# Kernel tuning notes

Measured on AMD Instinct MI355X. Metric: run time of the kernel, lower is better.

The kernel has to match this reference:

```python
import jax, jax.numpy as jnp
import numpy as np

D_KEY = 512
D_VALUE = 512
D_MEM_HIDDEN = 64
BATCH = 65536


def setup_inputs() -> dict:
    key = jax.random.key(0)
    ks = jax.random.split(key, 6)
    return {
        "key": jax.random.normal(ks[0], (BATCH, D_KEY), dtype=jnp.float32),
        "value": jax.random.normal(ks[1], (BATCH, D_VALUE), dtype=jnp.float32),
        # memory MLP weights (the stored memory)
        "mem_W1": jax.random.normal(ks[2], (D_MEM_HIDDEN, D_KEY), dtype=jnp.float32) * 0.02,
        "mem_b1": jnp.zeros((D_MEM_HIDDEN,), dtype=jnp.float32),
        "mem_W2": jax.random.normal(ks[3], (D_VALUE, D_MEM_HIDDEN), dtype=jnp.float32) * 0.02,
        "mem_b2": jnp.zeros((D_VALUE,), dtype=jnp.float32),
        # per-dimension precision head
        "prec_W": jax.random.normal(ks[4], (D_VALUE, D_KEY), dtype=jnp.float32) * 0.01,
        "prec_b": jnp.ones((D_VALUE,), dtype=jnp.float32),
    }


def reference(key, value, mem_W1, mem_b1, mem_W2, mem_b2, prec_W, prec_b):
    """Faithful translation of MemoryModule.free_energy.

    F = prec * clamp(value - pred, -3, 3)^2 - log(prec), averaged over d_value.
    """
    # predict: two-layer MLP with exact (erf) GELU, matching torch F.gelu default
    h = jax.nn.gelu(key @ mem_W1.T + mem_b1, approximate=False)  # (B, H)
    pred = h @ mem_W2.T + mem_b2                                  # (B, Dv)
    # precision head: softplus + 0.01, always positive
    prec = jax.nn.softplus(key @ prec_W.T + prec_b) + 0.01        # (B, Dv)
    error = jnp.clip(value - pred, -3.0, 3.0)                     # (B, Dv)
    F_per_dim = prec * error * error - jnp.log(prec)
    F_scalar = F_per_dim.mean(axis=-1)                            # (B,)
    return (F_scalar, pred, prec, error)
```

## Files before the change

kernel.cpp:

```cpp
#include <hip/hip_runtime.h>
#include <hip/hip_bf16.h>

#define BATCH 65536
#define DK 512
#define DV 512
#define DH 64
#define BM 64
#define NT (DV / 16)

typedef __attribute__((ext_vector_type(8))) short bf16x8;
typedef __attribute__((ext_vector_type(4))) float f32x4;

__device__ short g_wb[327680];

__device__ __forceinline__ short f2bf(float f) {
    union { __hip_bfloat16 h; short s; } u;
    u.h = __float2bfloat16(f);
    return u.s;
}

__global__ __launch_bounds__(256) void conv_weights(
    const float* __restrict__ W1, const float* __restrict__ W2,
    const float* __restrict__ Wp)
{
    int t = blockIdx.x * 256 + threadIdx.x;
    long bx = (long)t * 16;
    long inseg; const float* src; int sh;
    if (bx < 65536)       { inseg = bx;          src = W1; sh = 10; }
    else if (bx < 131072) { inseg = bx - 65536;  src = W2; sh = 7;  }
    else                  { inseg = bx - 131072; src = Wp; sh = 10; }
    long so = inseg ^ (((inseg >> sh) & 7) << 4);
    const float* p = src + (so >> 1);
    float4 a = *reinterpret_cast<const float4*>(p);
    float4 b = *reinterpret_cast<const float4*>(p + 4);
    bf16x8 r;
    r[0] = f2bf(a.x); r[1] = f2bf(a.y); r[2] = f2bf(a.z); r[3] = f2bf(a.w);
    r[4] = f2bf(b.x); r[5] = f2bf(b.y); r[6] = f2bf(b.z); r[7] = f2bf(b.w);
    *reinterpret_cast<bf16x8*>(reinterpret_cast<char*>(g_wb) + bx) = r;
}

__device__ __forceinline__ void gld16(const short* g, short* l) {
    __builtin_amdgcn_global_load_lds(
        (const __attribute__((address_space(1))) void*)g,
        (__attribute__((address_space(3))) void*)l, 16, 0, 0);
}

#define WPA 0
#define WPB 16384
#define W2A 32768
#define W2B (32768 + 2048)

__global__ __launch_bounds__(256, 4) void fused_free_energy(
    const float* __restrict__ key, const float* __restrict__ value,
    const float* __restrict__ b1, const float* __restrict__ b2,
    const float* __restrict__ pb,
    float* __restrict__ outF, float* __restrict__ outPred,
    float* __restrict__ outPrec, float* __restrict__ outErr)
{
    __shared__ __align__(16) short ldsS[18432];
    char* ldsb = reinterpret_cast<char*>(ldsS);

    const short* W1b = g_wb;
    const short* W2b = g_wb + 32768;
    const short* Wpb = g_wb + 65536;

    const int tid  = threadIdx.x;
    const int wave = tid >> 6;
    const int lane = tid & 63;
    const int lh   = lane & 15;
    const int lg   = lane >> 4;
    const long row0 = (long)blockIdx.x * BM;

    bf16x8 kreg[16];
    #pragma unroll
    for (int c = 0; c < 2; ++c) {
        const float4* kin = reinterpret_cast<const float4*>(key + (row0 + c * 32) * DK);
        #pragma unroll
        for (int i = 0; i < 16; ++i) {
            int idx = i * 256 + tid;
            int r = idx >> 7, c4 = idx & 127;
            float4 v = kin[idx];
            short4 s;
            s.x = f2bf(v.x); s.y = f2bf(v.y); s.z = f2bf(v.z); s.w = f2bf(v.w);
            int byte = (r * 1024 + c4 * 8) ^ ((r & 7) << 4);
            *reinterpret_cast<short4*>(ldsb + byte) = s;
        }
        __syncthreads();
        if ((wave >> 1) == c) {
            int rr = (wave & 1) * 16 + lh;
            #pragma unroll
            for (int kk = 0; kk < 16; ++kk) {
                int byte = (rr * 1024 + kk * 64 + lg * 16) ^ ((rr & 7) << 4);
                kreg[kk] = *reinterpret_cast<const bf16x8*>(ldsb + byte);
            }
        }
        __syncthreads();
    }

    const f32x4 zf = {0.f, 0.f, 0.f, 0.f};

    short hs_all[16];
    {
        #pragma unroll
        for (int i = 0; i < 4; ++i) {
            int ch = (wave + i * 4) * 1024;
            gld16(W1b + ((ch + lane * 16) >> 1), ldsS + ((WPA + ch) >> 1));
        }
        __syncthreads();
        #pragma unroll
        for (int jt = 0; jt < 4; ++jt) {
            char* cbuf = ldsb + ((jt & 1) ? WPB : WPA);
            if (jt < 3) {
                int nb_ = (jt & 1) ? WPA : WPB;
                #pragma unroll
                for (int i = 0; i < 4; ++i) {
                    int ch = (wave + i * 4) * 1024;
                    gld16(W1b + (((jt + 1) * 16384 + ch + lane * 16) >> 1),
                          ldsS + ((nb_ + ch) >> 1));
                }
            }
            f32x4 acc = zf;
            #pragma unroll
            for (int kk = 0; kk < 16; ++kk) {
                int byte = (lh * 1024 + kk * 64 + lg * 16) ^ ((lh & 7) << 4);
                bf16x8 af = *reinterpret_cast<const bf16x8*>(cbuf + byte);
                acc = __builtin_amdgcn_mfma_f32_16x16x32_bf16(af, kreg[kk], acc, 0, 0, 0);
            }
            float4 b1v = *reinterpret_cast<const float4*>(b1 + jt * 16 + lg * 4);
            float b1a[4] = {b1v.x, b1v.y, b1v.z, b1v.w};
            #pragma unroll
            for (int r = 0; r < 4; ++r) {
                float z = acc[r] + b1a[r];
                float g = 0.5f * z * (1.0f + erff(z * 0.70710678f));
                hs_all[jt * 4 + r] = f2bf(g);
            }
            __syncthreads();
        }
        #pragma unroll
        for (int jt = 0; jt < 4; ++jt) {
            int hb = WPA + wave * 2048 + ((lh * 128 + jt * 32 + lg * 8) ^ ((lh & 7) << 4));
            short4 hv = {hs_all[jt * 4 + 0], hs_all[jt * 4 + 1],
                         hs_all[jt * 4 + 2], hs_all[jt * 4 + 3]};
            *reinterpret_cast<short4*>(ldsb + hb) = hv;
        }
        __syncthreads();
    }

    bf16x8 hreg[2];
    #pragma unroll
    for (int kh = 0; kh < 2; ++kh) {
        int byte = (lh * 128 + kh * 64 + lg * 16) ^ ((lh & 7) << 4);
        hreg[kh] = *reinterpret_cast<const bf16x8*>(ldsb + WPA + wave * 2048 + byte);
    }
    __syncthreads();

    {
        #pragma unroll
        for (int i = 0; i < 4; ++i) {
            int ch = (wave + i * 4) * 1024;
            gld16(Wpb + ((ch + lane * 16) >> 1), ldsS + ((WPA + ch) >> 1));
        }
        if (wave < 2)
            gld16(W2b + ((wave * 1024 + lane * 16) >> 1), ldsS + ((W2A + wave * 1024) >> 1));
        __syncthreads();

        float facc = 0.f;
        const long grow = row0 + wave * 16 + lh;
        const float* vrow = value + grow * DV;
        float* prow = outPred + grow * DV;
        float* crow = outPrec + grow * DV;
        float* erow = outErr  + grow * DV;

        for (int it = 0; it < NT; ++it) {
            char* wpc = ldsb + ((it & 1) ? WPB : WPA);
            char* w2c = ldsb + ((it & 1) ? W2B : W2A);

            if (it + 1 < NT) {
                int nwp = (it & 1) ? WPA : WPB;
                int nw2 = (it & 1) ? W2A : W2B;
                #pragma unroll
                for (int i = 0; i < 4; ++i) {
                    int ch = (wave + i * 4) * 1024;
                    gld16(Wpb + (((it + 1) * 16384 + ch + lane * 16) >> 1),
                          ldsS + ((nwp + ch) >> 1));
                }
                if (wave < 2)
                    gld16(W2b + (((it + 1) * 2048 + wave * 1024 + lane * 16) >> 1),
                          ldsS + ((nw2 + wave * 1024) >> 1));
            }

            f32x4 acc3 = zf;
            #pragma unroll
            for (int kk = 0; kk < 16; ++kk) {
                int byte = (lh * 1024 + kk * 64 + lg * 16) ^ ((lh & 7) << 4);
                bf16x8 af = *reinterpret_cast<const bf16x8*>(wpc + byte);
                acc3 = __builtin_amdgcn_mfma_f32_16x16x32_bf16(af, kreg[kk], acc3, 0, 0, 0);
            }
            f32x4 acc2 = zf;
            #pragma unroll
            for (int kh = 0; kh < 2; ++kh) {
                int byte = (lh * 128 + kh * 64 + lg * 16) ^ ((lh & 7) << 4);
                bf16x8 af = *reinterpret_cast<const bf16x8*>(w2c + byte);
                acc2 = __builtin_amdgcn_mfma_f32_16x16x32_bf16(af, hreg[kh], acc2, 0, 0, 0);
            }

            int nb = it * 16 + lg * 4;
            float4 b2v = *reinterpret_cast<const float4*>(b2 + nb);
            float4 pbv = *reinterpret_cast<const float4*>(pb + nb);
            float4 val = *reinterpret_cast<const float4*>(vrow + nb);
            float b2a[4] = {b2v.x, b2v.y, b2v.z, b2v.w};
            float pba[4] = {pbv.x, pbv.y, pbv.z, pbv.w};
            float va[4]  = {val.x, val.y, val.z, val.w};
            float prv[4], pcv[4], erv[4];
            #pragma unroll
            for (int r = 0; r < 4; ++r) {
                float pred = acc2[r] + b2a[r];
                float z    = acc3[r] + pba[r];
                float prec = fmaxf(z, 0.f) + __logf(1.0f + __expf(-fabsf(z))) + 0.01f;
                float err  = fminf(fmaxf(va[r] - pred, -3.f), 3.f);
                prv[r] = pred; pcv[r] = prec; erv[r] = err;
                facc += prec * err * err - __logf(prec);
            }
            float4 pr4 = {prv[0], prv[1], prv[2], prv[3]};
            float4 pc4 = {pcv[0], pcv[1], pcv[2], pcv[3]};
            float4 er4 = {erv[0], erv[1], erv[2], erv[3]};
            *reinterpret_cast<float4*>(prow + nb) = pr4;
            *reinterpret_cast<float4*>(crow + nb) = pc4;
            *reinterpret_cast<float4*>(erow + nb) = er4;

            __syncthreads();
        }

        facc += __shfl_xor(facc, 16, 64);
        facc += __shfl_xor(facc, 32, 64);
        if (lane < 16) outF[grow] = facc * (1.0f / 512.0f);
    }
}

extern "C" void kernel_launch(void* const* d_in, const int* in_sizes, int n_in,
                              void* d_out, int out_size, void* d_ws, size_t ws_size,
                              hipStream_t stream) {
    const float* key   = (const float*)d_in[0];
    const float* value = (const float*)d_in[1];
    const float* W1    = (const float*)d_in[2];
    const float* b1    = (const float*)d_in[3];
    const float* W2    = (const float*)d_in[4];
    const float* b2    = (const float*)d_in[5];
    const float* Wp    = (const float*)d_in[6];
    const float* pb    = (const float*)d_in[7];

    float* outF    = (float*)d_out;
    float* outPred = outF + BATCH;
    float* outPrec = outPred + (long)BATCH * DV;
    float* outErr  = outPrec + (long)BATCH * DV;

    conv_weights<<<160, 256, 0, stream>>>(W1, W2, Wp);
    fused_free_energy<<<BATCH / BM, 256, 0, stream>>>(key, value, b1, b2, pb,
                                                      outF, outPred, outPrec, outErr);
}
```

Before: 289.3 us.

## Read bf16 weights directly from global/L2 instead of staging through LDS

The weight-staging pipeline through LDS is removed. Each wave now loads W1, Wp and W2 bf16 fragments straight from global memory, relying on L2/cache hits because every block shares the weights. This drops the per-iteration __syncthreads and the swizzled weight layout. Key rows are loaded directly into registers, the next value tile is prefetched, and the MFMA chains are split into two accumulators. Occupancy is lowered to 3 blocks per CU, and the change risks heavier global/L1 traffic since each wave re-fetches the weights independently.

```diff
diff --git a/kernel.cpp b/kernel.cpp
--- a/kernel.cpp
+++ b/kernel.cpp
@@ -11,7 +11,7 @@
 typedef __attribute__((ext_vector_type(8))) short bf16x8;
 typedef __attribute__((ext_vector_type(4))) float f32x4;
 
-__device__ short g_wb[327680];
+__device__ __align__(16) short g_wb[327680];
 
 __device__ __forceinline__ short f2bf(float f) {
     union { __hip_bfloat16 h; short s; } u;
@@ -19,46 +19,37 @@
     return u.s;
 }
 
+__device__ __forceinline__ bf16x8 pack8(float4 a, float4 b) {
+    bf16x8 r;
+    r[0] = f2bf(a.x); r[1] = f2bf(a.y); r[2] = f2bf(a.z); r[3] = f2bf(a.w);
+    r[4] = f2bf(b.x); r[5] = f2bf(b.y); r[6] = f2bf(b.z); r[7] = f2bf(b.w);
+    return r;
+}
+
 __global__ __launch_bounds__(256) void conv_weights(
     const float* __restrict__ W1, const float* __restrict__ W2,
     const float* __restrict__ Wp)
 {
     int t = blockIdx.x * 256 + threadIdx.x;
-    long bx = (long)t * 16;
-    long inseg; const float* src; int sh;
-    if (bx < 65536)       { inseg = bx;          src = W1; sh = 10; }
-    else if (bx < 131072) { inseg = bx - 65536;  src = W2; sh = 7;  }
-    else                  { inseg = bx - 131072; src = Wp; sh = 10; }
-    long so = inseg ^ (((inseg >> sh) & 7) << 4);
-    const float* p = src + (so >> 1);
-    float4 a = *reinterpret_cast<const float4*>(p);
-    float4 b = *reinterpret_cast<const float4*>(p + 4);
-    bf16x8 r;
-    r[0] = f2bf(a.x); r[1] = f2bf(a.y); r[2] = f2bf(a.z); r[3] = f2bf(a.w);
-    r[4] = f2bf(b.x); r[5] = f2bf(b.y); r[6] = f2bf(b.z); r[7] = f2bf(b.w);
-    *reinterpret_cast<bf16x8*>(reinterpret_cast<char*>(g_wb) + bx) = r;
+    long e = (long)t * 8;
+    const float* src; long off;
+    if (e < 32768)      { src = W1; off = e; }
+    else if (e < 65536) { src = W2; off = e - 32768; }
+    else                { src = Wp; off = e - 65536; }
+    float4 a = *reinterpret_cast<const float4*>(src + off);
+    float4 b = *reinterpret_cast<const float4*>(src + off + 4);
+    *reinterpret_cast<bf16x8*>(g_wb + e) = pack8(a, b);
 }
 
-__device__ __forceinline__ void gld16(const short* g, short* l) {
-    __builtin_amdgcn_global_load_lds(
-        (const __attribute__((address_space(1))) void*)g,
-        (__attribute__((address_space(3))) void*)l, 16, 0, 0);
-}
-
-#define WPA 0
-#define WPB 16384
-#define W2A 32768
-#define W2B (32768 + 2048)
-
-__global__ __launch_bounds__(256, 4) void fused_free_energy(
+__global__ __launch_bounds__(256, 3) void fused_free_energy(
     const float* __restrict__ key, const float* __restrict__ value,
     const float* __restrict__ b1, const float* __restrict__ b2,
     const float* __restrict__ pb,
     float* __restrict__ outF, float* __restrict__ outPred,
     float* __restrict__ outPrec, float* __restrict__ outErr)
 {
-    __shared__ __align__(16) short ldsS[18432];
-    char* ldsb = reinterpret_cast<char*>(ldsS);
+    __shared__ __align__(16) short hpark[4096];
+    char* hpb = reinterpret_cast<char*>(hpark);
 
     const short* W1b = g_wb;
     const short* W2b = g_wb + 32768;
@@ -70,100 +61,56 @@
     const int lh   = lane & 15;
     const int lg   = lane >> 4;
     const long row0 = (long)blockIdx.x * BM;
+    const f32x4 zf = {0.f, 0.f, 0.f, 0.f};
 
     bf16x8 kreg[16];
-    #pragma unroll
-    for (int c = 0; c < 2; ++c) {
-        const float4* kin = reinterpret_cast<const float4*>(key + (row0 + c * 32) * DK);
+    {
+        const float* krow = key + (row0 + wave * 16 + lh) * DK + lg * 8;
         #pragma unroll
-        for (int i = 0; i < 16; ++i) {
-            int idx = i * 256 + tid;
-            int r = idx >> 7, c4 = idx & 127;
-            float4 v = kin[idx];
-            short4 s;
-            s.x = f2bf(v.x); s.y = f2bf(v.y); s.z = f2bf(v.z); s.w = f2bf(v.w);
-            int byte = (r * 1024 + c4 * 8) ^ ((r & 7) << 4);
-            *reinterpret_cast<short4*>(ldsb + byte) = s;
+        for (int kk = 0; kk < 16; ++kk) {
+            float4 a = *reinterpret_cast<const float4*>(krow + kk * 32);
+            float4 b = *reinterpret_cast<const float4*>(krow + kk * 32 + 4);
+            kreg[kk] = pack8(a, b);
         }
-        __syncthreads();
-        if ((wave >> 1) == c) {
-            int rr = (wave & 1) * 16 + lh;
-            #pragma unroll
-            for (int kk = 0; kk < 16; ++kk) {
-                int byte = (rr * 1024 + kk * 64 + lg * 16) ^ ((rr & 7) << 4);
-                kreg[kk] = *reinterpret_cast<const bf16x8*>(ldsb + byte);
-            }
-        }
-        __syncthreads();
     }
 
-    const f32x4 zf = {0.f, 0.f, 0.f, 0.f};
-
     short hs_all[16];
-    {
+    #pragma unroll
+    for (int jt = 0; jt < 4; ++jt) {
+        const short* wt = W1b + (jt * 16 + lh) * DK + lg * 8;
+        f32x4 aE = zf, aO = zf;
         #pragma unroll
-        for (int i = 0; i < 4; ++i) {
-            int ch = (wave + i * 4) * 1024;
-            gld16(W1b + ((ch + lane * 16) >> 1), ldsS + ((WPA + ch) >> 1));
+        for (int kk = 0; kk < 16; kk += 2) {
+            bf16x8 f0 = *reinterpret_cast<const bf16x8*>(wt + kk * 32);
+            bf16x8 f1 = *reinterpret_cast<const bf16x8*>(wt + kk * 32 + 32);
+            aE = __builtin_amdgcn_mfma_f32_16x16x32_bf16(f0, kreg[kk],     aE, 0, 0, 0);
+            aO = __builtin_amdgcn_mfma_f32_16x16x32_bf16(f1, kreg[kk + 1], aO, 0, 0, 0);
         }
-        __syncthreads();
+        float4 b1v = *reinterpret_cast<const float4*>(b1 + jt * 16 + lg * 4);
+        float b1a[4] = {b1v.x, b1v.y, b1v.z, b1v.w};
         #pragma unroll
-        for (int jt = 0; jt < 4; ++jt) {
-            char* cbuf = ldsb + ((jt & 1) ? WPB : WPA);
-            if (jt < 3) {
-                int nb_ = (jt & 1) ? WPA : WPB;
-                #pragma unroll
-                for (int i = 0; i < 4; ++i) {
-                    int ch = (wave + i * 4) * 1024;
-                    gld16(W1b + (((jt + 1) * 16384 + ch + lane * 16) >> 1),
-                          ldsS + ((nb_ + ch) >> 1));
-                }
-            }
-            f32x4 acc = zf;
-            #pragma unroll
-            for (int kk = 0; kk < 16; ++kk) {
-                int byte = (lh * 1024 + kk * 64 + lg * 16) ^ ((lh & 7) << 4);
-                bf16x8 af = *reinterpret_cast<const bf16x8*>(cbuf + byte);
-                acc = __builtin_amdgcn_mfma_f32_16x16x32_bf16(af, kreg[kk], acc, 0, 0, 0);
-            }
-            float4 b1v = *reinterpret_cast<const float4*>(b1 + jt * 16 + lg * 4);
-            float b1a[4] = {b1v.x, b1v.y, b1v.z, b1v.w};
-            #pragma unroll
-            for (int r = 0; r < 4; ++r) {
-                float z = acc[r] + b1a[r];
-                float g = 0.5f * z * (1.0f + erff(z * 0.70710678f));
-                hs_all[jt * 4 + r] = f2bf(g);
-            }
-            __syncthreads();
+        for (int r = 0; r < 4; ++r) {
+            float z = aE[r] + aO[r] + b1a[r];
+            float g = 0.5f * z * (1.0f + erff(z * 0.70710678f));
+            hs_all[jt * 4 + r] = f2bf(g);
         }
-        #pragma unroll
-        for (int jt = 0; jt < 4; ++jt) {
-            int hb = WPA + wave * 2048 + ((lh * 128 + jt * 32 + lg * 8) ^ ((lh & 7) << 4));
-            short4 hv = {hs_all[jt * 4 + 0], hs_all[jt * 4 + 1],
-                         hs_all[jt * 4 + 2], hs_all[jt * 4 + 3]};
-            *reinterpret_cast<short4*>(ldsb + hb) = hv;
-        }
-        __syncthreads();
     }
-
+    #pragma unroll
+    for (int jt = 0; jt < 4; ++jt) {
+        int hb = wave * 2048 + ((lh * 128 + jt * 32 + lg * 8) ^ ((lh & 7) << 4));
+        short4 hv = {hs_all[jt * 4 + 0], hs_all[jt * 4 + 1],
+                     hs_all[jt * 4 + 2], hs_all[jt * 4 + 3]};
+        *reinterpret_cast<short4*>(hpb + hb) = hv;
+    }
+    __syncthreads();
     bf16x8 hreg[2];
     #pragma unroll
     for (int kh = 0; kh < 2; ++kh) {
         int byte = (lh * 128 + kh * 64 + lg * 16) ^ ((lh & 7) << 4);
-        hreg[kh] = *reinterpret_cast<const bf16x8*>(ldsb + WPA + wave * 2048 + byte);
+        hreg[kh] = *reinterpret_cast<const bf16x8*>(hpb + wave * 2048 + byte);
     }
-    __syncthreads();
 
     {
-        #pragma unroll
-        for (int i = 0; i < 4; ++i) {
-            int ch = (wave + i * 4) * 1024;
-            gld16(Wpb + ((ch + lane * 16) >> 1), ldsS + ((WPA + ch) >> 1));
-        }
-        if (wave < 2)
-            gld16(W2b + ((wave * 1024 + lane * 16) >> 1), ldsS + ((W2A + wave * 1024) >> 1));
-        __syncthreads();
-
         float facc = 0.f;
         const long grow = row0 + wave * 16 + lh;
         const float* vrow = value + grow * DV;
@@ -171,51 +118,43 @@
         float* crow = outPrec + grow * DV;
         float* erow = outErr  + grow * DV;
 
+        float4 vcur = *reinterpret_cast<const float4*>(vrow + lg * 4);
+
         for (int it = 0; it < NT; ++it) {
-            char* wpc = ldsb + ((it & 1) ? WPB : WPA);
-            char* w2c = ldsb + ((it & 1) ? W2B : W2A);
+            int nb = it * 16 + lg * 4;
 
-            if (it + 1 < NT) {
-                int nwp = (it & 1) ? WPA : WPB;
-                int nw2 = (it & 1) ? W2A : W2B;
-                #pragma unroll
-                for (int i = 0; i < 4; ++i) {
-                    int ch = (wave + i * 4) * 1024;
-                    gld16(Wpb + (((it + 1) * 16384 + ch + lane * 16) >> 1),
-                          ldsS + ((nwp + ch) >> 1));
-                }
-                if (wave < 2)
-                    gld16(W2b + (((it + 1) * 2048 + wave * 1024 + lane * 16) >> 1),
-                          ldsS + ((nw2 + wave * 1024) >> 1));
+            float4 vnx;
+            if (it + 1 < NT)
+                vnx = *reinterpret_cast<const float4*>(vrow + nb + 16);
+
+            const short* wt = Wpb + ((long)it * 16 + lh) * DK + lg * 8;
+            f32x4 aE = zf, aO = zf;
+            #pragma unroll
+            for (int kk = 0; kk < 16; kk += 2) {
+                bf16x8 f0 = *reinterpret_cast<const bf16x8*>(wt + kk * 32);
+                bf16x8 f1 = *reinterpret_cast<const bf16x8*>(wt + kk * 32 + 32);
+                aE = __builtin_amdgcn_mfma_f32_16x16x32_bf16(f0, kreg[kk],     aE, 0, 0, 0);
+                aO = __builtin_amdgcn_mfma_f32_16x16x32_bf16(f1, kreg[kk + 1], aO, 0, 0, 0);
             }
-
-            f32x4 acc3 = zf;
-            #pragma unroll
-            for (int kk = 0; kk < 16; ++kk) {
-                int byte = (lh * 1024 + kk * 64 + lg * 16) ^ ((lh & 7) << 4);
-                bf16x8 af = *reinterpret_cast<const bf16x8*>(wpc + byte);
-                acc3 = __builtin_amdgcn_mfma_f32_16x16x32_bf16(af, kreg[kk], acc3, 0, 0, 0);
-            }
+            const short* w2t = W2b + ((long)it * 16 + lh) * DH + lg * 8;
             f32x4 acc2 = zf;
             #pragma unroll
             for (int kh = 0; kh < 2; ++kh) {
-                int byte = (lh * 128 + kh * 64 + lg * 16) ^ ((lh & 7) << 4);
-                bf16x8 af = *reinterpret_cast<const bf16x8*>(w2c + byte);
-                acc2 = __builtin_amdgcn_mfma_f32_16x16x32_bf16(af, hreg[kh], acc2, 0, 0, 0);
+                bf16x8 f = *reinterpret_cast<const bf16x8*>(w2t + kh * 32);
+                acc2 = __builtin_amdgcn_mfma_f32_16x16x32_bf16(f, hreg[kh], acc2, 0, 0, 0);
             }
 
-            int nb = it * 16 + lg * 4;
             float4 b2v = *reinterpret_cast<const float4*>(b2 + nb);
             float4 pbv = *reinterpret_cast<const float4*>(pb + nb);
-            float4 val = *reinterpret_cast<const float4*>(vrow + nb);
             float b2a[4] = {b2v.x, b2v.y, b2v.z, b2v.w};
             float pba[4] = {pbv.x, pbv.y, pbv.z, pbv.w};
-            float va[4]  = {val.x, val.y, val.z, val.w};
+            float va[4]  = {vcur.x, vcur.y, vcur.z, vcur.w};
             float prv[4], pcv[4], erv[4];
             #pragma unroll
             for (int r = 0; r < 4; ++r) {
-                float pred = acc2[r] + b2a[r];
-                float z    = acc3[r] + pba[r];
+                float pred = aE[r] + aO[r] + pba[r];
+                float z    = pred;
+                pred = acc2[r] + b2a[r];
                 float prec = fmaxf(z, 0.f) + __logf(1.0f + __expf(-fabsf(z))) + 0.01f;
                 float err  = fminf(fmaxf(va[r] - pred, -3.f), 3.f);
                 prv[r] = pred; pcv[r] = prec; erv[r] = err;
@@ -228,7 +167,7 @@
             *reinterpret_cast<float4*>(crow + nb) = pc4;
             *reinterpret_cast<float4*>(erow + nb) = er4;
 
-            __syncthreads();
+            vcur = vnx;
         }
 
         facc += __shfl_xor(facc, 16, 64);
```

Result: slower. 418.5 us (+44.6%).
